# Kernel optimization log

Hardware: AMD Instinct MI355X
Metric: run time of the kernel (lower is better)

## Reference

```python
import jax, jax.numpy as jnp
import numpy as np

B, S, D, H = 2, 2048, 1024, 16
HD = D // H
EPS = 1e-5


def layer_norm(x, g, b):
    mu = jnp.mean(x, axis=-1, keepdims=True)
    var = jnp.mean(jnp.square(x - mu), axis=-1, keepdims=True)
    return (x - mu) * jax.lax.rsqrt(var + EPS) * g + b


def setup_inputs() -> dict:
    key = jax.random.key(0)
    ks = jax.random.split(key, 10)
    s = 0.02
    return {
        'x': jax.random.normal(ks[0], (B, S, D), jnp.float32),
        'Wq': jax.random.normal(ks[1], (D, D), jnp.float32) * s,
        'bq': jnp.zeros((D,), jnp.float32),
        'Wk': jax.random.normal(ks[2], (D, D), jnp.float32) * s,
        'bk': jnp.zeros((D,), jnp.float32),
        'Wv': jax.random.normal(ks[3], (D, D), jnp.float32) * s,
        'bv': jnp.zeros((D,), jnp.float32),
        'W1': jax.random.normal(ks[4], (D, 4 * D), jnp.float32) * s,
        'b1': jnp.zeros((4 * D,), jnp.float32),
        'W2': jax.random.normal(ks[5], (4 * D, D), jnp.float32) * s,
        'b2': jnp.zeros((D,), jnp.float32),
        'g1': jnp.ones((D,), jnp.float32),
        'be1': jnp.zeros((D,), jnp.float32),
        'g2': jnp.ones((D,), jnp.float32),
        'be2': jnp.zeros((D,), jnp.float32),
    }


def reference(x, Wq, bq, Wk, bk, Wv, bv, W1, b1, W2, b2, g1, be1, g2, be2):
    b, s, d = x.shape
    # QKV projections, split heads: [B,H,S,HD]
    Q = (x @ Wq + bq).reshape(b, s, H, HD).transpose(0, 2, 1, 3)
    K = (x @ Wk + bk).reshape(b, s, H, HD).transpose(0, 2, 1, 3)
    V = (x @ Wv + bv).reshape(b, s, H, HD).transpose(0, 2, 1, 3)
    score = jnp.einsum('bhqd,bhkd->bhqk', Q, K) / jnp.sqrt(jnp.float32(HD))
    attn = jax.nn.softmax(score, axis=-1)
    out = jnp.einsum('bhqk,bhkd->bhqd', attn, V)
    out = out.transpose(0, 2, 1, 3).reshape(b, s, d)
    # dropout(p=0.1) is identity in eval mode
    out = layer_norm(out + x, g1, be1)
    ffn = jax.nn.gelu(out @ W1 + b1, approximate=False) @ W2 + b2
    # NOTE: faithful to source: norm2(output + output), i.e. 2*ffn_out
    return layer_norm(ffn + ffn, g2, be2)
```

## Files before the change

### kernel.cpp

```cpp
#include <hip/hip_runtime.h>
#include <hip/hip_bf16.h>

typedef __hip_bfloat16 bf16;
typedef __attribute__((ext_vector_type(8))) short short8;
typedef __attribute__((ext_vector_type(4))) float floatx4;

struct __align__(8) bf16x4 { bf16 v[4]; };

#define LOG2E 1.4426950408889634f

__device__ __forceinline__ void gload_lds16(const void* g, void* l) {
  __builtin_amdgcn_global_load_lds(
      (const __attribute__((address_space(1))) void*)g,
      (__attribute__((address_space(3))) void*)l, 16, 0, 0);
}

__device__ __forceinline__ floatx4 mfma16(short8 a, short8 b, floatx4 c) {
  return __builtin_amdgcn_mfma_f32_16x16x32_bf16(a, b, c, 0, 0, 0);
}

__global__ __launch_bounds__(256) void convert_x(const float* __restrict__ x,
                                                 bf16* __restrict__ xb) {
  int i = blockIdx.x * 256 + threadIdx.x;
  float4 v = ((const float4*)x)[i];
  bf16x4 o;
  o.v[0] = __float2bfloat16(v.x);
  o.v[1] = __float2bfloat16(v.y);
  o.v[2] = __float2bfloat16(v.z);
  o.v[3] = __float2bfloat16(v.w);
  ((bf16x4*)xb)[i] = o;
}

__global__ __launch_bounds__(256) void transpose_w(const float* __restrict__ W,
                                                   bf16* __restrict__ WT,
                                                   int K, int N) {
  __shared__ float t[64][65];
  const int n0 = blockIdx.x * 64, k0 = blockIdx.y * 64;
  const int tid = threadIdx.x;
#pragma unroll
  for (int i = 0; i < 16; ++i) {
    int idx = i * 256 + tid;
    int r = idx >> 6, c = idx & 63;
    t[r][c] = W[(size_t)(k0 + r) * N + n0 + c];
  }
  __syncthreads();
#pragma unroll
  for (int i = 0; i < 16; ++i) {
    int idx = i * 256 + tid;
    int r = idx >> 6, c = idx & 63;
    WT[(size_t)(n0 + r) * K + k0 + c] = __float2bfloat16(t[c][r]);
  }
}

__global__ __launch_bounds__(256) void transpose_v(const bf16* __restrict__ V,
                                                   bf16* __restrict__ Vt) {
  __shared__ bf16 t[64][72];
  const int bh = blockIdx.y;
  const int s0 = blockIdx.x * 64;
  const bf16* src = V + (size_t)bh * 2048 * 64;
  bf16* dst = Vt + (size_t)bh * 64 * 2048;
  const int tid = threadIdx.x;
#pragma unroll
  for (int i = 0; i < 16; ++i) {
    int idx = i * 256 + tid;
    int r = idx >> 6, c = idx & 63;
    t[r][c] = src[(size_t)(s0 + r) * 64 + c];
  }
  __syncthreads();
#pragma unroll
  for (int i = 0; i < 16; ++i) {
    int idx = i * 256 + tid;
    int r = idx >> 6, c = idx & 63;
    dst[(size_t)r * 2048 + s0 + c] = t[c][r];
  }
}

template <int MODE>
__global__ __launch_bounds__(256, 2) void gemm_bt(
    const bf16* __restrict__ A, const bf16* __restrict__ BT,
    const float* __restrict__ bias0, const float* __restrict__ bias1,
    const float* __restrict__ bias2, void* __restrict__ C0,
    void* __restrict__ C1, void* __restrict__ C2,
    int M, int N, int K, int lda, int ldb) {
  __shared__ bf16 As[2][128 * 64];
  __shared__ bf16 Bs[2][128 * 64];
  const int tid = threadIdx.x;
  const int wid = tid >> 6, lane = tid & 63;
  const int l16 = lane & 15, lhi = lane >> 4;
  const int nwg = gridDim.x * gridDim.y;
  const int orig = blockIdx.y * gridDim.x + blockIdx.x;
  const int wflat = (orig & 7) * (nwg >> 3) + (orig >> 3);
  const int bx = wflat % gridDim.x, by = wflat / gridDim.x;
  const int brow = by * 128, bcol = bx * 128;
  const int z = blockIdx.z;
  const size_t koff = (size_t)z * (size_t)K;
  const int wr = (wid >> 1) * 64, wc = (wid & 1) * 64;
  const int swz = (l16 & 7) << 4;
  floatx4 acc[4][4] = {};

  auto stage = [&](int buf, int kt) {
#pragma unroll
    for (int i = 0; i < 4; ++i) {
      const int f = i * 256 + tid;
      const int row = f >> 3;
      const int cb = ((f & 7) * 16) ^ ((row & 7) << 4);
      gload_lds16((const char*)A + ((size_t)(brow + row) * lda + koff + kt) * 2 + cb,
                  (char*)&As[buf][0] + (size_t)f * 16);
      gload_lds16((const char*)BT + ((size_t)(bcol + row) * ldb + koff + kt) * 2 + cb,
                  (char*)&Bs[buf][0] + (size_t)f * 16);
    }
  };

  const int nk = K >> 6;
  stage(0, 0);
  int cur = 0;
  for (int t = 0; t < nk; ++t) {
    if (t + 1 < nk) {
      stage(cur ^ 1, (t + 1) << 6);
      asm volatile("s_waitcnt vmcnt(8)" ::: "memory");
    } else {
      asm volatile("s_waitcnt vmcnt(0)" ::: "memory");
    }
    asm volatile("s_barrier" ::: "memory");
#pragma unroll
    for (int kk = 0; kk < 2; ++kk) {
      short8 af[4], bfr[4];
#pragma unroll
      for (int m = 0; m < 4; ++m)
        af[m] = *(const short8*)((const char*)&As[cur][0] +
                                 (wr + m * 16 + l16) * 128 + ((kk * 64 + lhi * 16) ^ swz));
#pragma unroll
      for (int n = 0; n < 4; ++n)
        bfr[n] = *(const short8*)((const char*)&Bs[cur][0] +
                                  (wc + n * 16 + l16) * 128 + ((kk * 64 + lhi * 16) ^ swz));
      __builtin_amdgcn_s_setprio(1);
#pragma unroll
      for (int m = 0; m < 4; ++m)
#pragma unroll
        for (int n = 0; n < 4; ++n) acc[m][n] = mfma16(af[m], bfr[n], acc[m][n]);
      __builtin_amdgcn_s_setprio(0);
    }
    asm volatile("s_barrier" ::: "memory");
    cur ^= 1;
  }

#pragma unroll
  for (int m = 0; m < 4; ++m) {
    const int rowb = brow + wr + m * 16 + lhi * 4;
#pragma unroll
    for (int n = 0; n < 4; ++n) {
      const int col = bcol + wc + n * 16 + l16;
#pragma unroll
      for (int r = 0; r < 4; ++r) {
        float v = acc[m][n][r];
        const int gr = rowb + r;
        if constexpr (MODE == 0) {
          const int which = col >> 10;
          const int nl = col & 1023;
          const float* bp = (which == 0) ? bias0 : (which == 1) ? bias1 : bias2;
          v += bp[nl];
          const int b = gr >> 11, s = gr & 2047;
          const int h = nl >> 6, hd = nl & 63;
          const size_t dst = ((size_t)(b * 16 + h) * 2048 + s) * 64 + hd;
          bf16* out = (which == 0) ? (bf16*)C0 : (which == 1) ? (bf16*)C1 : (bf16*)C2;
          out[dst] = __float2bfloat16(v);
        } else if constexpr (MODE == 1) {
          v += bias0[col];
          float gchar = 0.5f * v * (1.0f + erff(v * 0.70710678118654752f));
          ((bf16*)C0)[(size_t)gr * N + col] = __float2bfloat16(gchar);
        } else if constexpr (MODE == 2) {
          v += bias0[col];
          ((float*)C0)[(size_t)gr * N + col] = v;
        } else {
          float* dst = (z == 0) ? (float*)C0 : (float*)C1;
          dst[(size_t)gr * N + col] = v;
        }
      }
    }
  }
}

__global__ __launch_bounds__(512, 2) void flash_attn(const bf16* __restrict__ Q,
                                                     const bf16* __restrict__ Kb,
                                                     const bf16* __restrict__ Vt,
                                                     bf16* __restrict__ attn) {
  __shared__ bf16 Ks[2][64 * 64];
  __shared__ bf16 Vs[2][64 * 64];
  __shared__ bf16 Ps[8][16 * 64];
  const int tid = threadIdx.x, wid = tid >> 6, lane = tid & 63;
  const int l16 = lane & 15, lhi = lane >> 4, lhi4 = (lane >> 4) * 4;
  const int bid = blockIdx.x;
  const int w = (bid & 7) * 64 + (bid >> 3);
  const int bh = w >> 4, qtile = w & 15;
  const bf16* Qbh = Q + (size_t)bh * 2048 * 64;
  const char* Kbh = (const char*)(Kb + (size_t)bh * 2048 * 64);
  const char* Vbh = (const char*)(Vt + (size_t)bh * 64 * 2048);
  bf16* Pw = &Ps[wid][0];
  const int q0 = qtile * 128 + wid * 16;
  const int swA = (l16 & 7) << 3;
  const int swzB = (l16 & 7) << 4;

  const int strow = tid >> 3;
  const int stcol = ((tid & 7) * 16) ^ ((strow & 7) << 4);

  short8 qf[2];
#pragma unroll
  for (int kk = 0; kk < 2; ++kk)
    qf[kk] = *(const short8*)&Qbh[(size_t)(q0 + l16) * 64 + kk * 32 + lhi * 8];

  floatx4 o[4] = {};
  float mrow = -1e30f;
  float lrow = 0.0f;
  const float SC = 0.125f * LOG2E;

  auto stage = [&](bf16* Kd, bf16* Vd, int t) {
    const int kvr = t * 64;
    gload_lds16(Kbh + (size_t)(kvr + strow) * 128 + stcol, (char*)Kd + tid * 16);
    gload_lds16(Vbh + (size_t)strow * 4096 + (size_t)kvr * 2 + stcol, (char*)Vd + tid * 16);
  };

  auto tile = [&](bf16* Kc, bf16* Vc, bf16* Kn, bf16* Vn, int t) {
    if (t + 1 < 32) {
      stage(Kn, Vn, t + 1);
      asm volatile("s_waitcnt vmcnt(2)" ::: "memory");
    } else {
      asm volatile("s_waitcnt vmcnt(0)" ::: "memory");
    }
    asm volatile("s_barrier" ::: "memory");

    short8 kf[2][4];
#pragma unroll
    for (int kk = 0; kk < 2; ++kk)
#pragma unroll
      for (int fc = 0; fc < 4; ++fc)
        kf[kk][fc] = *(const short8*)((const char*)Kc + (fc * 16 + l16) * 128 +
                                      ((kk * 64 + lhi * 16) ^ swzB));

    floatx4 sf[4] = {};
    __builtin_amdgcn_s_setprio(1);
#pragma unroll
    for (int kk = 0; kk < 2; ++kk)
#pragma unroll
      for (int fc = 0; fc < 4; ++fc) sf[fc] = mfma16(kf[kk][fc], qf[kk], sf[fc]);
    __builtin_amdgcn_s_setprio(0);

    {
      float a0 = fmaxf(fmaxf(sf[0][0], sf[0][1]), fmaxf(sf[0][2], sf[0][3]));
      float a1 = fmaxf(fmaxf(sf[1][0], sf[1][1]), fmaxf(sf[1][2], sf[1][3]));
      float a2 = fmaxf(fmaxf(sf[2][0], sf[2][1]), fmaxf(sf[2][2], sf[2][3]));
      float a3 = fmaxf(fmaxf(sf[3][0], sf[3][1]), fmaxf(sf[3][2], sf[3][3]));
      float mx = fmaxf(fmaxf(a0, a1), fmaxf(a2, a3));
      mx = fmaxf(mx, __shfl_xor(mx, 16));
      mx = fmaxf(mx, __shfl_xor(mx, 32));
      mx *= SC;
      if (__any(mx > mrow + 11.54f)) {
        const float mnew = fmaxf(mrow, mx);
        const float corr = exp2f(mrow - mnew);
        mrow = mnew;
        lrow *= corr;
#pragma unroll
        for (int r = 0; r < 4; ++r) {
          const float c = __shfl(corr, lhi4 + r);
#pragma unroll
          for (int fc = 0; fc < 4; ++fc) o[fc][r] *= c;
        }
      }
      const float m = mrow;
      float rs = 0.0f;
#pragma unroll
      for (int fc = 0; fc < 4; ++fc)
#pragma unroll
        for (int r = 0; r < 4; ++r) {
          const float p = exp2f(fmaf(sf[fc][r], SC, -m));
          sf[fc][r] = p;
          rs += p;
        }
      rs += __shfl_xor(rs, 16);
      rs += __shfl_xor(rs, 32);
      lrow += rs;
#pragma unroll
      for (int fc = 0; fc < 4; ++fc) {
        bf16x4 pk;
#pragma unroll
        for (int r = 0; r < 4; ++r) pk.v[r] = __float2bfloat16(sf[fc][r]);
        *(bf16x4*)&Pw[l16 * 64 + ((fc * 16 + lhi4) ^ swA)] = pk;
      }
    }

    short8 pf[2];
#pragma unroll
    for (int kk = 0; kk < 2; ++kk)
      pf[kk] = *(const short8*)&Pw[l16 * 64 + ((kk * 32 + lhi * 8) ^ swA)];
    __builtin_amdgcn_s_setprio(1);
#pragma unroll
    for (int kk = 0; kk < 2; ++kk) {
      short8 vf[4];
#pragma unroll
      for (int fc = 0; fc < 4; ++fc)
        vf[fc] = *(const short8*)((const char*)Vc + (fc * 16 + l16) * 128 +
                                  ((kk * 64 + lhi * 16) ^ swzB));
#pragma unroll
      for (int fc = 0; fc < 4; ++fc) o[fc] = mfma16(pf[kk], vf[fc], o[fc]);
    }
    __builtin_amdgcn_s_setprio(0);

    asm volatile("s_barrier" ::: "memory");
  };

  stage(&Ks[0][0], &Vs[0][0], 0);
  for (int t = 0; t < 32; t += 2) {
    tile(&Ks[0][0], &Vs[0][0], &Ks[1][0], &Vs[1][0], t);
    tile(&Ks[1][0], &Vs[1][0], &Ks[0][0], &Vs[0][0], t + 1);
  }

  const int b = bh >> 4, h = bh & 15;
#pragma unroll
  for (int r = 0; r < 4; ++r) {
    const float lr = __shfl(lrow, lhi4 + r);
    const float inv = 1.0f / lr;
    const int s = q0 + lhi4 + r;
    const size_t rowbase = (size_t)(b * 2048 + s) * 1024 + h * 64;
#pragma unroll
    for (int fc = 0; fc < 4; ++fc)
      attn[rowbase + fc * 16 + l16] = __float2bfloat16(o[fc][r] * inv);
  }
}

__global__ __launch_bounds__(256) void ln_res(const bf16* __restrict__ attn,
                                              const float* __restrict__ x,
                                              const float* __restrict__ g,
                                              const float* __restrict__ be,
                                              bf16* __restrict__ out) {
  __shared__ float sa[4], sb[4];
  const int row = blockIdx.x;
  const size_t base = (size_t)row * 1024;
  const int tid = threadIdx.x;
  const int c0 = tid * 4;
  float4 xv = *(const float4*)(x + base + c0);
  bf16x4 av = *(const bf16x4*)(attn + base + c0);
  float v[4];
  v[0] = xv.x + __bfloat162float(av.v[0]);
  v[1] = xv.y + __bfloat162float(av.v[1]);
  v[2] = xv.z + __bfloat162float(av.v[2]);
  v[3] = xv.w + __bfloat162float(av.v[3]);
  float s = v[0] + v[1] + v[2] + v[3];
  float ss = v[0]*v[0] + v[1]*v[1] + v[2]*v[2] + v[3]*v[3];
#pragma unroll
  for (int d = 32; d > 0; d >>= 1) { s += __shfl_down(s, d); ss += __shfl_down(ss, d); }
  const int wid = tid >> 6, lane = tid & 63;
  if (lane == 0) { sa[wid] = s; sb[wid] = ss; }
  __syncthreads();
  if (tid == 0) { sa[0] = sa[0]+sa[1]+sa[2]+sa[3]; sb[0] = sb[0]+sb[1]+sb[2]+sb[3]; }
  __syncthreads();
  s = sa[0]; ss = sb[0];
  const float mu = s * (1.0f / 1024.0f);
  const float var = ss * (1.0f / 1024.0f) - mu * mu;
  const float rs = rsqrtf(var + 1e-5f);
  float4 gv = *(const float4*)(g + c0);
  float4 bv = *(const float4*)(be + c0);
  bf16x4 o;
  o.v[0] = __float2bfloat16((v[0]-mu)*rs*gv.x + bv.x);
  o.v[1] = __float2bfloat16((v[1]-mu)*rs*gv.y + bv.y);
  o.v[2] = __float2bfloat16((v[2]-mu)*rs*gv.z + bv.z);
  o.v[3] = __float2bfloat16((v[3]-mu)*rs*gv.w + bv.w);
  *(bf16x4*)(out + base + c0) = o;
}

__global__ __launch_bounds__(256) void ln2_kernel(const float* __restrict__ y0,
                                                  const float* __restrict__ y1,
                                                  const float* __restrict__ b2,
                                                  const float* __restrict__ g,
                                                  const float* __restrict__ be,
                                                  float* __restrict__ out) {
  __shared__ float sa[4], sb[4];
  const int row = blockIdx.x;
  const size_t base = (size_t)row * 1024;
  const int tid = threadIdx.x;
  const int c0 = tid * 4;
  float4 ya = *(const float4*)(y0 + base + c0);
  float4 yb = *(const float4*)(y1 + base + c0);
  float4 bb = *(const float4*)(b2 + c0);
  float v[4] = {2.0f * (ya.x + yb.x + bb.x), 2.0f * (ya.y + yb.y + bb.y),
                2.0f * (ya.z + yb.z + bb.z), 2.0f * (ya.w + yb.w + bb.w)};
  float s = v[0] + v[1] + v[2] + v[3];
  float ss = v[0]*v[0] + v[1]*v[1] + v[2]*v[2] + v[3]*v[3];
#pragma unroll
  for (int d = 32; d > 0; d >>= 1) { s += __shfl_down(s, d); ss += __shfl_down(ss, d); }
  const int wid = tid >> 6, lane = tid & 63;
  if (lane == 0) { sa[wid] = s; sb[wid] = ss; }
  __syncthreads();
  if (tid == 0) { sa[0] = sa[0]+sa[1]+sa[2]+sa[3]; sb[0] = sb[0]+sb[1]+sb[2]+sb[3]; }
  __syncthreads();
  s = sa[0]; ss = sb[0];
  const float mu = s * (1.0f / 1024.0f);
  const float var = ss * (1.0f / 1024.0f) - mu * mu;
  const float rs = rsqrtf(var + 1e-5f);
  float4 gv = *(const float4*)(g + c0);
  float4 bv = *(const float4*)(be + c0);
  float4 o;
  o.x = (v[0]-mu)*rs*gv.x + bv.x;
  o.y = (v[1]-mu)*rs*gv.y + bv.y;
  o.z = (v[2]-mu)*rs*gv.z + bv.z;
  o.w = (v[3]-mu)*rs*gv.w + bv.w;
  *(float4*)(out + base + c0) = o;
}

extern "C" void kernel_launch(void* const* d_in, const int* in_sizes, int n_in,
                              void* d_out, int out_size, void* d_ws, size_t ws_size,
                              hipStream_t stream) {
  const float* x   = (const float*)d_in[0];
  const float* Wq  = (const float*)d_in[1];
  const float* bq  = (const float*)d_in[2];
  const float* Wk  = (const float*)d_in[3];
  const float* bk  = (const float*)d_in[4];
  const float* Wv  = (const float*)d_in[5];
  const float* bv  = (const float*)d_in[6];
  const float* W1  = (const float*)d_in[7];
  const float* b1  = (const float*)d_in[8];
  const float* W2  = (const float*)d_in[9];
  const float* b2  = (const float*)d_in[10];
  const float* g1  = (const float*)d_in[11];
  const float* be1 = (const float*)d_in[12];
  const float* g2  = (const float*)d_in[13];
  const float* be2 = (const float*)d_in[14];

  char* ws = (char*)d_ws;
  bf16* xb    = (bf16*)(ws + 0ull);
  bf16* WqkvT = (bf16*)(ws + 8388608ull);
  bf16* W1T   = (bf16*)(ws + 14680064ull);
  bf16* W2T   = (bf16*)(ws + 23068672ull);
  bf16* Qb    = (bf16*)(ws + 31457280ull);
  bf16* Kb    = (bf16*)(ws + 39845888ull);
  bf16* Vb    = (bf16*)(ws + 48234496ull);
  bf16* Vt    = (bf16*)(ws + 56623104ull);
  bf16* h1    = (bf16*)(ws + 31457280ull);
  bf16* attn  = (bf16*)(ws + 65011712ull);
  bf16* ln1   = (bf16*)(ws + 73400320ull);
  float* y2a  = (float*)(ws + 0ull);
  float* y2b  = (float*)(ws + 65011712ull);
  float* out  = (float*)d_out;

  convert_x<<<4096, 256, 0, stream>>>(x, xb);
  transpose_w<<<dim3(16, 16), 256, 0, stream>>>(Wq, WqkvT, 1024, 1024);
  transpose_w<<<dim3(16, 16), 256, 0, stream>>>(Wk, WqkvT + 1024 * 1024, 1024, 1024);
  transpose_w<<<dim3(16, 16), 256, 0, stream>>>(Wv, WqkvT + 2 * 1024 * 1024, 1024, 1024);
  transpose_w<<<dim3(64, 16), 256, 0, stream>>>(W1, W1T, 1024, 4096);
  transpose_w<<<dim3(16, 64), 256, 0, stream>>>(W2, W2T, 4096, 1024);

  gemm_bt<0><<<dim3(24, 32), 256, 0, stream>>>(xb, WqkvT, bq, bk, bv,
                                               (void*)Qb, (void*)Kb, (void*)Vb,
                                               4096, 3072, 1024, 1024, 1024);
  transpose_v<<<dim3(32, 32), 256, 0, stream>>>(Vb, Vt);
  flash_attn<<<512, 512, 0, stream>>>(Qb, Kb, Vt, attn);
  ln_res<<<4096, 256, 0, stream>>>(attn, x, g1, be1, ln1);
  gemm_bt<1><<<dim3(32, 32), 256, 0, stream>>>(ln1, W1T, b1, nullptr, nullptr,
                                               (void*)h1, nullptr, nullptr,
                                               4096, 4096, 1024, 1024, 1024);
  gemm_bt<3><<<dim3(8, 32, 2), 256, 0, stream>>>(h1, W2T, nullptr, nullptr, nullptr,
                                                 (void*)y2a, (void*)y2b, nullptr,
                                                 4096, 1024, 2048, 4096, 4096);
  ln2_kernel<<<4096, 256, 0, stream>>>(y2a, y2b, b2, g2, be2, out);
}
```

Baseline: 249.2 us.

## Add 256x256-tile 8-wave GEMM for QKV and FFN1 projections

Introduces a new gemm256 kernel with 256x256 output tiles, 512 threads (8 waves in a 2x4 layout), a double-buffered swizzled LDS, and a k-loop split into interleaved fragment-load and MFMA phases. The QKV and FFN-up GEMMs now use it. The goal is higher arithmetic intensity per LDS/global byte and fewer workgroups. The cost is 128 KB of LDS per block and 128 accumulator registers per lane, which lowers occupancy, and there are few blocks (192 and 256) relative to the CU count, so the tail may be poor.

```diff
diff --git a/kernel.cpp b/kernel.cpp
--- a/kernel.cpp
+++ b/kernel.cpp
@@ -72,6 +72,140 @@
     int idx = i * 256 + tid;
     int r = idx >> 6, c = idx & 63;
     dst[(size_t)r * 2048 + s0 + c] = t[c][r];
+  }
+}
+
+template <int MODE>
+__global__ __launch_bounds__(512, 2) void gemm256(
+    const bf16* __restrict__ A, const bf16* __restrict__ BT,
+    const float* __restrict__ bias0, const float* __restrict__ bias1,
+    const float* __restrict__ bias2, void* __restrict__ C0,
+    void* __restrict__ C1, void* __restrict__ C2,
+    int M, int N, int K, int lda, int ldb) {
+  __shared__ bf16 As[2][256 * 64];
+  __shared__ bf16 Bs[2][256 * 64];
+  const int tid = threadIdx.x;
+  const int lane = tid & 63, wid = tid >> 6;
+  const int l16 = lane & 15, lhi = lane >> 4;
+  const int wm = wid >> 2, wn = wid & 3;
+  const int nwg = gridDim.x * gridDim.y;
+  const int orig = blockIdx.y * gridDim.x + blockIdx.x;
+  const int wflat = (orig & 7) * (nwg >> 3) + (orig >> 3);
+  const int bx = wflat % gridDim.x, by = wflat / gridDim.x;
+  const int brow = by * 256, bcol = bx * 256;
+  const int swz = (l16 & 7) << 4;
+  floatx4 acc[8][4] = {};
+
+  auto stage = [&](int buf, int kt) {
+#pragma unroll
+    for (int i = 0; i < 4; ++i) {
+      const int f = i * 512 + tid;
+      const int row = f >> 3;
+      const int cb = ((f & 7) * 16) ^ ((row & 7) << 4);
+      gload_lds16((const char*)A + ((size_t)(brow + row) * lda + kt) * 2 + cb,
+                  (char*)&As[buf][0] + (size_t)f * 16);
+    }
+#pragma unroll
+    for (int i = 0; i < 4; ++i) {
+      const int f = i * 512 + tid;
+      const int row = f >> 3;
+      const int cb = ((f & 7) * 16) ^ ((row & 7) << 4);
+      gload_lds16((const char*)BT + ((size_t)(bcol + row) * ldb + kt) * 2 + cb,
+                  (char*)&Bs[buf][0] + (size_t)f * 16);
+    }
+  };
+
+  const int nk = K >> 6;
+  stage(0, 0);
+  asm volatile("s_waitcnt vmcnt(0)" ::: "memory");
+  asm volatile("s_barrier" ::: "memory");
+  int cur = 0;
+  for (int t = 0; t < nk; ++t) {
+    const char* Ab = (const char*)&As[cur][0];
+    const char* Bb = (const char*)&Bs[cur][0];
+    short8 af[8], b0, b1;
+#pragma unroll
+    for (int m = 0; m < 8; ++m)
+      af[m] = *(const short8*)(Ab + (wm * 128 + m * 16 + l16) * 128 + ((lhi * 16) ^ swz));
+    b0 = *(const short8*)(Bb + (wn * 64 + l16) * 128 + ((lhi * 16) ^ swz));
+    b1 = *(const short8*)(Bb + (wn * 64 + 16 + l16) * 128 + ((lhi * 16) ^ swz));
+    if (t + 1 < nk) stage(cur ^ 1, (t + 1) << 6);
+    asm volatile("s_barrier" ::: "memory");
+    __builtin_amdgcn_s_setprio(1);
+#pragma unroll
+    for (int m = 0; m < 8; ++m) {
+      acc[m][0] = mfma16(af[m], b0, acc[m][0]);
+      acc[m][1] = mfma16(af[m], b1, acc[m][1]);
+    }
+    __builtin_amdgcn_s_setprio(0);
+    asm volatile("s_barrier" ::: "memory");
+    b0 = *(const short8*)(Bb + (wn * 64 + 32 + l16) * 128 + ((lhi * 16) ^ swz));
+    b1 = *(const short8*)(Bb + (wn * 64 + 48 + l16) * 128 + ((lhi * 16) ^ swz));
+    asm volatile("s_barrier" ::: "memory");
+    __builtin_amdgcn_s_setprio(1);
+#pragma unroll
+    for (int m = 0; m < 8; ++m) {
+      acc[m][2] = mfma16(af[m], b0, acc[m][2]);
+      acc[m][3] = mfma16(af[m], b1, acc[m][3]);
+    }
+    __builtin_amdgcn_s_setprio(0);
+    asm volatile("s_barrier" ::: "memory");
+#pragma unroll
+    for (int m = 0; m < 8; ++m)
+      af[m] = *(const short8*)(Ab + (wm * 128 + m * 16 + l16) * 128 + ((64 + lhi * 16) ^ swz));
+    b0 = *(const short8*)(Bb + (wn * 64 + l16) * 128 + ((64 + lhi * 16) ^ swz));
+    b1 = *(const short8*)(Bb + (wn * 64 + 16 + l16) * 128 + ((64 + lhi * 16) ^ swz));
+    asm volatile("s_barrier" ::: "memory");
+    __builtin_amdgcn_s_setprio(1);
+#pragma unroll
+    for (int m = 0; m < 8; ++m) {
+      acc[m][0] = mfma16(af[m], b0, acc[m][0]);
+      acc[m][1] = mfma16(af[m], b1, acc[m][1]);
+    }
+    __builtin_amdgcn_s_setprio(0);
+    asm volatile("s_barrier" ::: "memory");
+    b0 = *(const short8*)(Bb + (wn * 64 + 32 + l16) * 128 + ((64 + lhi * 16) ^ swz));
+    b1 = *(const short8*)(Bb + (wn * 64 + 48 + l16) * 128 + ((64 + lhi * 16) ^ swz));
+    asm volatile("s_waitcnt vmcnt(0)" ::: "memory");
+    asm volatile("s_barrier" ::: "memory");
+    __builtin_amdgcn_s_setprio(1);
+#pragma unroll
+    for (int m = 0; m < 8; ++m) {
+      acc[m][2] = mfma16(af[m], b0, acc[m][2]);
+      acc[m][3] = mfma16(af[m], b1, acc[m][3]);
+    }
+    __builtin_amdgcn_s_setprio(0);
+    asm volatile("s_barrier" ::: "memory");
+    cur ^= 1;
+  }
+
+#pragma unroll
+  for (int m = 0; m < 8; ++m) {
+    const int rowb = brow + wm * 128 + m * 16 + lhi * 4;
+#pragma unroll
+    for (int n = 0; n < 4; ++n) {
+      const int col = bcol + wn * 64 + n * 16 + l16;
+#pragma unroll
+      for (int r = 0; r < 4; ++r) {
+        float v = acc[m][n][r];
+        const int gr = rowb + r;
+        if constexpr (MODE == 0) {
+          const int which = col >> 10;
+          const int nl = col & 1023;
+          const float* bp = (which == 0) ? bias0 : (which == 1) ? bias1 : bias2;
+          v += bp[nl];
+          const int b = gr >> 11, s = gr & 2047;
+          const int h = nl >> 6, hd = nl & 63;
+          const size_t dst = ((size_t)(b * 16 + h) * 2048 + s) * 64 + hd;
+          bf16* out = (which == 0) ? (bf16*)C0 : (which == 1) ? (bf16*)C1 : (bf16*)C2;
+          out[dst] = __float2bfloat16(v);
+        } else {
+          v += bias0[col];
+          float gch = 0.5f * v * (1.0f + erff(v * 0.70710678118654752f));
+          ((bf16*)C0)[(size_t)gr * N + col] = __float2bfloat16(gch);
+        }
+      }
+    }
   }
 }
 
@@ -154,27 +288,8 @@
       for (int r = 0; r < 4; ++r) {
         float v = acc[m][n][r];
         const int gr = rowb + r;
-        if constexpr (MODE == 0) {
-          const int which = col >> 10;
-          const int nl = col & 1023;
-          const float* bp = (which == 0) ? bias0 : (which == 1) ? bias1 : bias2;
-          v += bp[nl];
-          const int b = gr >> 11, s = gr & 2047;
-          const int h = nl >> 6, hd = nl & 63;
-          const size_t dst = ((size_t)(b * 16 + h) * 2048 + s) * 64 + hd;
-          bf16* out = (which == 0) ? (bf16*)C0 : (which == 1) ? (bf16*)C1 : (bf16*)C2;
-          out[dst] = __float2bfloat16(v);
-        } else if constexpr (MODE == 1) {
-          v += bias0[col];
-          float gchar = 0.5f * v * (1.0f + erff(v * 0.70710678118654752f));
-          ((bf16*)C0)[(size_t)gr * N + col] = __float2bfloat16(gchar);
-        } else if constexpr (MODE == 2) {
-          v += bias0[col];
-          ((float*)C0)[(size_t)gr * N + col] = v;
-        } else {
-          float* dst = (z == 0) ? (float*)C0 : (float*)C1;
-          dst[(size_t)gr * N + col] = v;
-        }
+        float* dst = (z == 0) ? (float*)C0 : (float*)C1;
+        dst[(size_t)gr * N + col] = v;
       }
     }
   }
@@ -447,13 +562,13 @@
   transpose_w<<<dim3(64, 16), 256, 0, stream>>>(W1, W1T, 1024, 4096);
   transpose_w<<<dim3(16, 64), 256, 0, stream>>>(W2, W2T, 4096, 1024);
 
-  gemm_bt<0><<<dim3(24, 32), 256, 0, stream>>>(xb, WqkvT, bq, bk, bv,
+  gemm256<0><<<dim3(12, 16), 512, 0, stream>>>(xb, WqkvT, bq, bk, bv,
                                                (void*)Qb, (void*)Kb, (void*)Vb,
                                                4096, 3072, 1024, 1024, 1024);
   transpose_v<<<dim3(32, 32), 256, 0, stream>>>(Vb, Vt);
   flash_attn<<<512, 512, 0, stream>>>(Qb, Kb, Vt, attn);
   ln_res<<<4096, 256, 0, stream>>>(attn, x, g1, be1, ln1);
-  gemm_bt<1><<<dim3(32, 32), 256, 0, stream>>>(ln1, W1T, b1, nullptr, nullptr,
+  gemm256<1><<<dim3(16, 16), 512, 0, stream>>>(ln1, W1T, b1, nullptr, nullptr,
                                                (void*)h1, nullptr, nullptr,
                                                4096, 4096, 1024, 1024, 1024);
   gemm_bt<3><<<dim3(8, 32, 2), 256, 0, stream>>>(h1, W2T, nullptr, nullptr, nullptr,
```

Result: faster. 244.0 us (-2.1%).
